# Performance work log

Measured on AMD Instinct MI355X. Metric: run time of the kernel, lower is better.

Reference implementation:

```python
import jax, jax.numpy as jnp
import numpy as np

B, C, N, L = 32, 256, 1024, 12
H = 8
DK = C // H  # 32


def setup_inputs() -> dict:
    key = jax.random.key(0)
    ks = jax.random.split(key, 8)
    inp = {
        "input": jax.random.normal(ks[0], (B, C, N, L), dtype=jnp.float32),
        # 1x1 conv weights stored as [out_ch, in_ch] (kernel is 1x1)
        "q_w": jax.random.normal(ks[1], (C, C), dtype=jnp.float32) * 0.02,
        "q_b": jnp.zeros((C,), dtype=jnp.float32),
        "v_w": jax.random.normal(ks[2], (C, C), dtype=jnp.float32) * 0.02,
        "v_b": jnp.zeros((C,), dtype=jnp.float32),
        "c_w": jax.random.normal(ks[3], (C, C), dtype=jnp.float32) * 0.02,
        "c_b": jnp.zeros((C,), dtype=jnp.float32),
        # xavier_uniform_: bound = sqrt(6/(fan_in+fan_out)) over last two dims
        "s_bank": jax.random.uniform(ks[4], (H, L, N, DK), dtype=jnp.float32,
                                      minval=-1.0, maxval=1.0) * np.float32(np.sqrt(6.0 / (N + DK))),
    }
    return inp


def _conv1x1_relu(x, w, b):
    # x: [B, Cin, N, L], w: [Cout, Cin] -> [B, Cout, N, L]; dropout is eval-mode identity
    return jax.nn.relu(jnp.einsum('oi,binl->bonl', w, x) + b[None, :, None, None])


def reference(input, q_w, q_b, v_w, v_b, c_w, c_b, s_bank):
    b, c, n, l = input.shape
    inv_sqrt_dk = np.float32(1.0 / np.sqrt(DK))

    q = _conv1x1_relu(input, q_w, q_b)   # [B, C, N, L]
    v = _conv1x1_relu(input, v_w, v_b)   # [B, C, N, L]

    def split_heads(t):
        # [B, C, N, L] -> [B, H, DK, N, L] -> [B, H, L, N, DK]
        return t.reshape(b, H, DK, n, l).transpose(0, 1, 4, 3, 2)

    query = jax.nn.softmax(split_heads(q) * inv_sqrt_dk, axis=-1)        # [B,H,L,N,DK]
    value = split_heads(v)                                               # [B,H,L,N,DK]
    key_ = jax.nn.softmax(s_bank[:, :, :n, :] * inv_sqrt_dk, axis=-1)    # [H,L,N,DK]

    kv = jnp.einsum('hlnx,bhlny->bhlxy', key_, value)      # [B,H,L,DK,DK]
    qkv = jnp.einsum('bhlnx,bhlxy->bhlny', query, kv)      # [B,H,L,N,DK]

    # [B,H,L,N,DK] -> [B,H,DK,N,L] -> [B,C,N,L]
    out = qkv.transpose(0, 1, 4, 3, 2).reshape(b, c, n, l)
    return _conv1x1_relu(out, c_w, c_b)
```

## Files before the change

kernel.cpp:

```cpp
#include <hip/hip_runtime.h>

#define B_   32
#define C_   256
#define N_   1024
#define L_   12
#define H_   8
#define DK_  32
#define NL_  12288
#define CNL_ 3145728
#define ND_  32768
#define HLN_ 98304
#define SCALE_ 0.17677669529663687f

typedef _Float16 half8 __attribute__((ext_vector_type(8)));
typedef _Float16 half4 __attribute__((ext_vector_type(4)));
typedef float f32x4 __attribute__((ext_vector_type(4)));

__device__ __forceinline__ int div12(int s) { return (int)(((unsigned)s * 43691u) >> 19); }
__device__ __forceinline__ int fsw(int c) { return c ^ (((c >> 4) & 1) << 2) ^ ((c >> 6) & 3); }

__global__ __launch_bounds__(256) void k_prep_softmax(
    const float* __restrict__ wq, const float* __restrict__ wv,
    const float* __restrict__ cw, const float* __restrict__ sb,
    _Float16* __restrict__ Wfrag, _Float16* __restrict__ Cfrag,
    _Float16* __restrict__ ksT) {
    __shared__ _Float16 smT[32 * 260];
    const int t = threadIdx.x;
    if (blockIdx.x < 96) {
        const int gid = blockIdx.x * 256 + t;
        if (gid < 16384) {
            const int kb = gid >> 11, r = gid & 2047;
            const int mt = r >> 6, o = (r >> 4) & 3, lo = r & 15;
            const int m = mt * 16 + lo;
            const float* src = (m < 256 ? wq + (size_t)m * 256 : wv + (size_t)(m - 256) * 256)
                               + kb * 32 + o * 8;
            f32x4 a0 = *(const f32x4*)src, a1 = *(const f32x4*)(src + 4);
            half8 h;
#pragma unroll
            for (int i = 0; i < 4; ++i) { h[i] = (_Float16)a0[i]; h[4 + i] = (_Float16)a1[i]; }
            *(half8*)(Wfrag + (size_t)gid * 8) = h;
        } else {
            const int c = gid - 16384;
            const int kb = c >> 10, r = c & 1023;
            const int mt = r >> 6, o = (r >> 4) & 3, lo = r & 15;
            const int m = mt * 16 + lo;
            const float* src = cw + (size_t)m * 256 + kb * 32 + o * 8;
            f32x4 a0 = *(const f32x4*)src, a1 = *(const f32x4*)(src + 4);
            half8 h;
#pragma unroll
            for (int i = 0; i < 4; ++i) { h[i] = (_Float16)a0[i]; h[4 + i] = (_Float16)a1[i]; }
            *(half8*)(Cfrag + (size_t)c * 8) = h;
        }
        return;
    }
    const int bx = blockIdx.x - 96;
    const int row = bx * 256 + t;
    const f32x4* src = (const f32x4*)(sb + (size_t)row * DK_);
    float v[DK_];
#pragma unroll
    for (int i = 0; i < 8; i++) {
        f32x4 t4 = src[i];
        v[4*i+0] = t4[0]; v[4*i+1] = t4[1]; v[4*i+2] = t4[2]; v[4*i+3] = t4[3];
    }
    float m = v[0];
#pragma unroll
    for (int i = 1; i < DK_; i++) m = fmaxf(m, v[i]);
    float s = 0.f;
#pragma unroll
    for (int i = 0; i < DK_; i++) { v[i] = __expf((v[i] - m) * SCALE_); s += v[i]; }
    const float inv = 1.f / s;
#pragma unroll
    for (int i = 0; i < DK_; i++) smT[i * 260 + t] = (_Float16)(v[i] * inv);
    __syncthreads();
    const int x = t >> 3, off = (t & 7) * 32;
    const int base = bx * 256;
    const int hl = base >> 10, nb = base & 1023;
    _Float16* dst = ksT + (size_t)hl * ND_ + (size_t)x * 1024 + nb + off;
    const _Float16* srcT = &smT[x * 260 + off];
#pragma unroll
    for (int k = 0; k < 4; ++k)
        *(half8*)(dst + k * 8) = *(const half8*)(srcT + k * 8);
}

__global__ __launch_bounds__(512, 2) void k_conv_qv(
    const float* __restrict__ x, const _Float16* __restrict__ Wfrag,
    const float* __restrict__ bqp, const float* __restrict__ bvp,
    _Float16* __restrict__ qh, _Float16* __restrict__ vh)
{
    __shared__ __align__(16) _Float16 Xl[2][8192];

    const int t = threadIdx.x;
    const int sgrp = blockIdx.x;
    const int b = blockIdx.y;
    const int sbase = sgrp * 768;
    const int w = t >> 6, lane = t & 63;
    const int lo = lane & 15, hi = lane >> 4;

    half8 af[8][4];
#pragma unroll
    for (int kb = 0; kb < 8; ++kb)
#pragma unroll
        for (int m = 0; m < 4; ++m)
            af[kb][m] = *(const half8*)(Wfrag +
                ((size_t)kb*2048 + (size_t)(w*4 + m)*64 + lane) * 8);

    const float* bsel = (w >= 4) ? bvp : bqp;
    f32x4 bb[4];
#pragma unroll
    for (int m = 0; m < 4; ++m)
        bb[m] = *(const f32x4*)(bsel + ((w & 3)*4 + m)*16 + hi*4);

    const int xch = t >> 1, xsh = (t & 1) * 8;
    const int g = xch >> 3, elem = xch & 7;
    const int wb = g*128 + elem;
    const int sx = xsh ^ ((g & 7) << 1) ^ (xsh >> 3);
    const float* px = x + (size_t)b * CNL_ + (size_t)xch * NL_ + sbase + xsh;

    const int base_r = hi*128 + ((lo ^ (hi*2) ^ ((lo & 8) >> 3)) << 3);

    f32x4 c0 = *(const f32x4*)px,        c1 = *(const f32x4*)(px + 4);
    f32x4 c2 = *(const f32x4*)(px + 16), c3 = *(const f32x4*)(px + 20);
#pragma unroll
    for (int k = 0; k < 4; ++k) {
        Xl[0][wb + (((k  ) ^ sx) << 3)]        = (_Float16)c0[k];
        Xl[0][wb + (((k+4) ^ sx) << 3)]        = (_Float16)c1[k];
        Xl[0][4096 + wb + (((k  ) ^ sx) << 3)] = (_Float16)c2[k];
        Xl[0][4096 + wb + (((k+4) ^ sx) << 3)] = (_Float16)c3[k];
    }
    c0 = *(const f32x4*)(px + 32); c1 = *(const f32x4*)(px + 36);
    c2 = *(const f32x4*)(px + 48); c3 = *(const f32x4*)(px + 52);

    for (int i = 0; i < 24; ++i) {
        asm volatile("s_waitcnt lgkmcnt(0)" ::: "memory");
        __builtin_amdgcn_s_barrier();
        __builtin_amdgcn_sched_barrier(0);
        if (i < 23) {
            _Float16* Xn = Xl[(i + 1) & 1];
#pragma unroll
            for (int k = 0; k < 4; ++k) {
                Xn[wb + (((k  ) ^ sx) << 3)]        = (_Float16)c0[k];
                Xn[wb + (((k+4) ^ sx) << 3)]        = (_Float16)c1[k];
                Xn[4096 + wb + (((k  ) ^ sx) << 3)] = (_Float16)c2[k];
                Xn[4096 + wb + (((k+4) ^ sx) << 3)] = (_Float16)c3[k];
            }
            if (i < 22) {
                const float* p = px + (size_t)(i + 2) * 32;
                c0 = *(const f32x4*)p;        c1 = *(const f32x4*)(p + 4);
                c2 = *(const f32x4*)(p + 16); c3 = *(const f32x4*)(p + 20);
            }
        }
        const _Float16* Xc = Xl[i & 1];
        f32x4 acc[4][2] = {};
#pragma unroll
        for (int kb = 0; kb < 8; ++kb) {
            const int ro = kb*512 + (base_r ^ ((kb & 1) << 6));
            half8 bf0 = *(const half8*)&Xc[ro];
            half8 bf1 = *(const half8*)&Xc[4096 + ro];
#pragma unroll
            for (int m = 0; m < 4; ++m) {
                acc[m][0] = __builtin_amdgcn_mfma_f32_16x16x32_f16(af[kb][m], bf0, acc[m][0], 0, 0, 0);
                acc[m][1] = __builtin_amdgcn_mfma_f32_16x16x32_f16(af[kb][m], bf1, acc[m][1], 0, 0, 0);
            }
        }
#pragma unroll
        for (int u = 0; u < 2; ++u) {
            const int sg = sbase + i*32 + u*16 + lo;
            const int n = div12(sg), l = sg - n*12;
#pragma unroll
            for (int m = 0; m < 4; ++m) {
                const int o = (w*4 + m)*16 + hi*4;
                const int ol = o & 255;
                _Float16* dst0 = (w >= 4) ? vh : qh;
                half4 hh;
#pragma unroll
                for (int r = 0; r < 4; ++r) hh[r] = (_Float16)fmaxf(acc[m][u][r] + bb[m][r], 0.f);
                *(half4*)(dst0 + ((size_t)(b*8 + (ol >> 5))*12 + l)*ND_ + (size_t)n*32 + (ol & 31)) = hh;
            }
        }
    }
}

__global__ __launch_bounds__(256) void k_kv(const _Float16* __restrict__ ksT,
    const _Float16* __restrict__ v, _Float16* __restrict__ kvT) {
    __shared__ float red[4096];
    const int bid = blockIdx.x;
    const int bh = bid / 12;
    const int l  = bid - bh * 12;
    const int h  = bh & 7;
    const int t = threadIdx.x, w = t >> 6, lane = t & 63;
    const int lo = lane & 15, hi = lane >> 4;
    const _Float16* vb  = v   + (size_t)bid * ND_;
    const _Float16* ksb = ksT + (size_t)(h*12 + l) * ND_;

    f32x4 acc[2][2] = {};
#pragma unroll 2
    for (int c = 0; c < 8; ++c) {
        const int n0 = w*256 + c*32 + hi*8;
        half8 a0, a1;
#pragma unroll
        for (int j = 0; j < 8; ++j) {
            a0[j] = vb[(size_t)(n0 + j)*32 + lo];
            a1[j] = vb[(size_t)(n0 + j)*32 + 16 + lo];
        }
        half8 b0 = *(const half8*)(ksb + (size_t)lo*1024 + n0);
        half8 b1 = *(const half8*)(ksb + (size_t)(16 + lo)*1024 + n0);
        acc[0][0] = __builtin_amdgcn_mfma_f32_16x16x32_f16(a0, b0, acc[0][0], 0, 0, 0);
        acc[0][1] = __builtin_amdgcn_mfma_f32_16x16x32_f16(a0, b1, acc[0][1], 0, 0, 0);
        acc[1][0] = __builtin_amdgcn_mfma_f32_16x16x32_f16(a1, b0, acc[1][0], 0, 0, 0);
        acc[1][1] = __builtin_amdgcn_mfma_f32_16x16x32_f16(a1, b1, acc[1][1], 0, 0, 0);
    }
#pragma unroll
    for (int m = 0; m < 2; ++m)
#pragma unroll
        for (int xm = 0; xm < 2; ++xm)
#pragma unroll
            for (int reg = 0; reg < 4; ++reg)
                red[w*1024 + (m*16 + hi*4 + reg)*32 + xm*16 + lo] = acc[m][xm][reg];
    __syncthreads();
    const int e = t * 4;
    f32x4 s = *(const f32x4*)&red[e];
    s += *(const f32x4*)&red[1024 + e];
    s += *(const f32x4*)&red[2048 + e];
    s += *(const f32x4*)&red[3072 + e];
    half4 o;
#pragma unroll
    for (int i = 0; i < 4; ++i) o[i] = (_Float16)s[i];
    *(half4*)(kvT + (size_t)bid * 1024 + e) = o;
}

__global__ __launch_bounds__(512, 2) void k_conv_out(
    const _Float16* __restrict__ q, const _Float16* __restrict__ kvw,
    const _Float16* __restrict__ Cfrag, const float* __restrict__ cbp,
    float* __restrict__ out) {
    __shared__ __align__(16) _Float16 Xt[2][6144];
    __shared__ float Cb[256];

    const int t = threadIdx.x;
    const int bx = blockIdx.x, b = blockIdx.y;
    const int s0 = bx * 192;
    const int n0 = bx * 16;
    const int w = t >> 6, lane = t & 63;
    const int lo = lane & 15, hi = lane >> 4;
    if (t < 64) *(f32x4*)&Cb[t*4] = *(const f32x4*)(cbp + t*4);

    f32x4 acc[4][6] = {};

    const bool pvw = (w < 6);
    const int li0 = w * 2;
    const int qrow = n0 + lo;
    const size_t hstep = (size_t)12 * ND_;
    const _Float16* qb_b = q + (size_t)b * 8 * hstep;
    const _Float16* kv_b = kvw + (size_t)b * 98304;

    half8 hq0 = {}, hq1 = {};
    if (pvw) {
        hq0 = *(const half8*)(qb_b + (size_t)li0 * ND_ + (size_t)qrow*32 + hi*8);
        hq1 = *(const half8*)(qb_b + (size_t)(li0+1) * ND_ + (size_t)qrow*32 + hi*8);
    }

    for (int ph = 0; ph <= 8; ++ph) {
        if (ph < 8 && pvw) {
            half8 nq0 = hq0, nq1 = hq1;
            if (ph < 7) {
                nq0 = *(const half8*)(qb_b + (ph+1)*hstep + (size_t)li0 * ND_ + (size_t)qrow*32 + hi*8);
                nq1 = *(const half8*)(qb_b + (ph+1)*hstep + (size_t)(li0+1) * ND_ + (size_t)qrow*32 + hi*8);
            }
            const _Float16* kvh = kv_b + (size_t)ph * 12288;
            _Float16* Xd = Xt[ph & 1];
#pragma unroll
            for (int sub = 0; sub < 2; ++sub) {
                const half8 hq = sub ? hq1 : hq0;
                const int li = li0 + sub;
                float qv[8];
#pragma unroll
                for (int i = 0; i < 8; ++i) qv[i] = (float)hq[i];
                float m8 = fmaxf(fmaxf(fmaxf(qv[0], qv[1]), fmaxf(qv[2], qv[3])),
                                 fmaxf(fmaxf(qv[4], qv[5]), fmaxf(qv[6], qv[7])));
                m8 = fmaxf(m8, __shfl_xor(m8, 16));
                m8 = fmaxf(m8, __shfl_xor(m8, 32));
                const float mS = m8 * SCALE_;
                float ex[8]; float ssum = 0.f;
#pragma unroll
                for (int i = 0; i < 8; ++i) { ex[i] = __expf(qv[i]*SCALE_ - mS); ssum += ex[i]; }
                ssum += __shfl_xor(ssum, 16);
                ssum += __shfl_xor(ssum, 32);
                const float pin = 1.f / ssum;
                half8 af;
#pragma unroll
                for (int i = 0; i < 8; ++i) af[i] = (_Float16)(ex[i] * pin);
                const half8 b0 = *(const half8*)(kvh + li*1024 + lo*32 + hi*8);
                const half8 b1 = *(const half8*)(kvh + li*1024 + (16+lo)*32 + hi*8);
                f32x4 d0 = {}, d1 = {};
                d0 = __builtin_amdgcn_mfma_f32_16x16x32_f16(af, b0, d0, 0, 0, 0);
                d1 = __builtin_amdgcn_mfma_f32_16x16x32_f16(af, b1, d1, 0, 0, 0);
#pragma unroll
                for (int reg = 0; reg < 4; ++reg) {
                    const int sr = (hi*4 + reg)*12 + li;
                    const int cb_ = (sr >> 4)*64 + (sr & 15);
                    const int ca = cb_ + (lo >> 3)*16;
                    const int cc = cb_ + (2 + (lo >> 3))*16;
                    Xd[fsw(ca)*8 + (lo & 7)] = (_Float16)d0[reg];
                    Xd[fsw(cc)*8 + (lo & 7)] = (_Float16)d1[reg];
                }
            }
            hq0 = nq0; hq1 = nq1;
        }
        if (ph >= 1) {
            const _Float16* Wk = Cfrag + (size_t)(ph - 1) * 8192;
            const _Float16* Xc = Xt[(ph - 1) & 1];
            half8 af2[4], bf[6];
#pragma unroll
            for (int m = 0; m < 4; ++m)
                af2[m] = *(const half8*)(Wk + ((((w>>1)*4 + m)*4 + hi)*16 + lo) * 8);
#pragma unroll
            for (int sf = 0; sf < 6; ++sf) {
                const int rc = ((w & 1)*6 + sf)*64 + hi*16 + lo;
                bf[sf] = *(const half8*)&Xc[fsw(rc)*8];
            }
#pragma unroll
            for (int m = 0; m < 4; ++m)
#pragma unroll
                for (int sf = 0; sf < 6; ++sf)
                    acc[m][sf] = __builtin_amdgcn_mfma_f32_16x16x32_f16(af2[m], bf[sf], acc[m][sf], 0, 0, 0);
        }
        asm volatile("s_waitcnt lgkmcnt(0)" ::: "memory");
        __builtin_amdgcn_s_barrier();
        __builtin_amdgcn_sched_barrier(0);
    }

#pragma unroll
    for (int m = 0; m < 4; ++m) {
        const int o = (w>>1)*64 + m*16 + hi*4;
        const f32x4 bb = *(const f32x4*)&Cb[o];
#pragma unroll
        for (int sf = 0; sf < 6; ++sf) {
            const int s = s0 + (w&1)*96 + sf*16 + lo;
            float* dst = out + (size_t)(b*256 + o)*12288 + s;
#pragma unroll
            for (int i = 0; i < 4; ++i)
                dst[(size_t)i * 12288] = fmaxf(acc[m][sf][i] + bb[i], 0.f);
        }
    }
}

extern "C" void kernel_launch(void* const* d_in, const int* in_sizes, int n_in,
                              void* d_out, int out_size, void* d_ws, size_t ws_size,
                              hipStream_t stream) {
    const float* input = (const float*)d_in[0];
    const float* q_w   = (const float*)d_in[1];
    const float* q_b   = (const float*)d_in[2];
    const float* v_w   = (const float*)d_in[3];
    const float* v_b   = (const float*)d_in[4];
    const float* c_w   = (const float*)d_in[5];
    const float* c_b   = (const float*)d_in[6];
    const float* s_bank= (const float*)d_in[7];
    float* out = (float*)d_out;

    char* ws = (char*)d_ws;
    _Float16* ks16 = (_Float16*)ws;
    _Float16* qh   = (_Float16*)(ws + 6291456);
    _Float16* vh   = qh + (size_t)100663296;
    _Float16* kvT  = vh + (size_t)100663296;
    _Float16* Wfrag= kvT + (size_t)3145728;
    _Float16* Cfrag= Wfrag + (size_t)131072;

    k_prep_softmax<<<dim3(96 + HLN_/256), dim3(256), 0, stream>>>(
        q_w, v_w, c_w, s_bank, Wfrag, Cfrag, ks16);
    k_conv_qv<<<dim3(16, 32), dim3(512), 0, stream>>>(input, Wfrag, q_b, v_b, qh, vh);
    k_kv<<<dim3(B_ * H_ * L_), dim3(256), 0, stream>>>(ks16, vh, kvT);
    k_conv_out<<<dim3(64, 32), dim3(512), 0, stream>>>(qh, kvT, Cfrag, c_b, out);
}
```

Baseline: 528.9 us.

## Deepen conv_qv global prefetch to two stages and give each kv wave its own slice

In the q/v projection kernel, global loads of the input tile are issued two iterations ahead, using two register sets that alternate with a 2x-unrolled loop, instead of one iteration ahead. The aim is to hide more global memory latency behind the MFMA work. In the kv kernel, each wave now computes a whole (b,h,l) slice across all of N, which removes the shared-memory cross-wave reduction and the __syncthreads. The grid shrinks to a quarter, and each wave writes its result directly with scattered half stores; the cost is more registers in conv_qv and longer serial loops per wave in kv.

```diff
diff --git a/kernel.cpp b/kernel.cpp
--- a/kernel.cpp
+++ b/kernel.cpp
@@ -118,35 +118,55 @@
 
     const int base_r = hi*128 + ((lo ^ (hi*2) ^ ((lo & 8) >> 3)) << 3);
 
-    f32x4 c0 = *(const f32x4*)px,        c1 = *(const f32x4*)(px + 4);
-    f32x4 c2 = *(const f32x4*)(px + 16), c3 = *(const f32x4*)(px + 20);
-#pragma unroll
-    for (int k = 0; k < 4; ++k) {
-        Xl[0][wb + (((k  ) ^ sx) << 3)]        = (_Float16)c0[k];
-        Xl[0][wb + (((k+4) ^ sx) << 3)]        = (_Float16)c1[k];
-        Xl[0][4096 + wb + (((k  ) ^ sx) << 3)] = (_Float16)c2[k];
-        Xl[0][4096 + wb + (((k+4) ^ sx) << 3)] = (_Float16)c3[k];
-    }
-    c0 = *(const f32x4*)(px + 32); c1 = *(const f32x4*)(px + 36);
-    c2 = *(const f32x4*)(px + 48); c3 = *(const f32x4*)(px + 52);
-
+    {
+        f32x4 t0 = *(const f32x4*)px,        t1 = *(const f32x4*)(px + 4);
+        f32x4 t2 = *(const f32x4*)(px + 16), t3 = *(const f32x4*)(px + 20);
+#pragma unroll
+        for (int k = 0; k < 4; ++k) {
+            Xl[0][wb + (((k  ) ^ sx) << 3)]        = (_Float16)t0[k];
+            Xl[0][wb + (((k+4) ^ sx) << 3)]        = (_Float16)t1[k];
+            Xl[0][4096 + wb + (((k  ) ^ sx) << 3)] = (_Float16)t2[k];
+            Xl[0][4096 + wb + (((k+4) ^ sx) << 3)] = (_Float16)t3[k];
+        }
+    }
+    f32x4 cB0 = *(const f32x4*)(px + 32), cB1 = *(const f32x4*)(px + 36);
+    f32x4 cB2 = *(const f32x4*)(px + 48), cB3 = *(const f32x4*)(px + 52);
+    f32x4 cA0 = *(const f32x4*)(px + 64), cA1 = *(const f32x4*)(px + 68);
+    f32x4 cA2 = *(const f32x4*)(px + 80), cA3 = *(const f32x4*)(px + 84);
+
+#pragma unroll 2
     for (int i = 0; i < 24; ++i) {
         asm volatile("s_waitcnt lgkmcnt(0)" ::: "memory");
         __builtin_amdgcn_s_barrier();
         __builtin_amdgcn_sched_barrier(0);
         if (i < 23) {
             _Float16* Xn = Xl[(i + 1) & 1];
-#pragma unroll
-            for (int k = 0; k < 4; ++k) {
-                Xn[wb + (((k  ) ^ sx) << 3)]        = (_Float16)c0[k];
-                Xn[wb + (((k+4) ^ sx) << 3)]        = (_Float16)c1[k];
-                Xn[4096 + wb + (((k  ) ^ sx) << 3)] = (_Float16)c2[k];
-                Xn[4096 + wb + (((k+4) ^ sx) << 3)] = (_Float16)c3[k];
-            }
-            if (i < 22) {
-                const float* p = px + (size_t)(i + 2) * 32;
-                c0 = *(const f32x4*)p;        c1 = *(const f32x4*)(p + 4);
-                c2 = *(const f32x4*)(p + 16); c3 = *(const f32x4*)(p + 20);
+            if ((i + 1) & 1) {
+#pragma unroll
+                for (int k = 0; k < 4; ++k) {
+                    Xn[wb + (((k  ) ^ sx) << 3)]        = (_Float16)cB0[k];
+                    Xn[wb + (((k+4) ^ sx) << 3)]        = (_Float16)cB1[k];
+                    Xn[4096 + wb + (((k  ) ^ sx) << 3)] = (_Float16)cB2[k];
+                    Xn[4096 + wb + (((k+4) ^ sx) << 3)] = (_Float16)cB3[k];
+                }
+                if (i < 21) {
+                    const float* p = px + (size_t)(i + 3) * 32;
+                    cB0 = *(const f32x4*)p;        cB1 = *(const f32x4*)(p + 4);
+                    cB2 = *(const f32x4*)(p + 16); cB3 = *(const f32x4*)(p + 20);
+                }
+            } else {
+#pragma unroll
+                for (int k = 0; k < 4; ++k) {
+                    Xn[wb + (((k  ) ^ sx) << 3)]        = (_Float16)cA0[k];
+                    Xn[wb + (((k+4) ^ sx) << 3)]        = (_Float16)cA1[k];
+                    Xn[4096 + wb + (((k  ) ^ sx) << 3)] = (_Float16)cA2[k];
+                    Xn[4096 + wb + (((k+4) ^ sx) << 3)] = (_Float16)cA3[k];
+                }
+                if (i < 21) {
+                    const float* p = px + (size_t)(i + 3) * 32;
+                    cA0 = *(const f32x4*)p;        cA1 = *(const f32x4*)(p + 4);
+                    cA2 = *(const f32x4*)(p + 16); cA3 = *(const f32x4*)(p + 20);
+                }
             }
         }
         const _Float16* Xc = Xl[i & 1];
@@ -182,20 +202,20 @@
 
 __global__ __launch_bounds__(256) void k_kv(const _Float16* __restrict__ ksT,
     const _Float16* __restrict__ v, _Float16* __restrict__ kvT) {
-    __shared__ float red[4096];
-    const int bid = blockIdx.x;
+    const int t = threadIdx.x;
+    const int wv = t >> 6, lane = t & 63;
+    const int bid = blockIdx.x * 4 + wv;
     const int bh = bid / 12;
     const int l  = bid - bh * 12;
     const int h  = bh & 7;
-    const int t = threadIdx.x, w = t >> 6, lane = t & 63;
     const int lo = lane & 15, hi = lane >> 4;
     const _Float16* vb  = v   + (size_t)bid * ND_;
     const _Float16* ksb = ksT + (size_t)(h*12 + l) * ND_;
 
     f32x4 acc[2][2] = {};
-#pragma unroll 2
-    for (int c = 0; c < 8; ++c) {
-        const int n0 = w*256 + c*32 + hi*8;
+#pragma unroll 4
+    for (int c = 0; c < 32; ++c) {
+        const int n0 = c*32 + hi*8;
         half8 a0, a1;
 #pragma unroll
         for (int j = 0; j < 8; ++j) {
@@ -209,23 +229,14 @@
         acc[1][0] = __builtin_amdgcn_mfma_f32_16x16x32_f16(a1, b0, acc[1][0], 0, 0, 0);
         acc[1][1] = __builtin_amdgcn_mfma_f32_16x16x32_f16(a1, b1, acc[1][1], 0, 0, 0);
     }
+    _Float16* dst = kvT + (size_t)bid * 1024;
 #pragma unroll
     for (int m = 0; m < 2; ++m)
 #pragma unroll
         for (int xm = 0; xm < 2; ++xm)
 #pragma unroll
             for (int reg = 0; reg < 4; ++reg)
-                red[w*1024 + (m*16 + hi*4 + reg)*32 + xm*16 + lo] = acc[m][xm][reg];
-    __syncthreads();
-    const int e = t * 4;
-    f32x4 s = *(const f32x4*)&red[e];
-    s += *(const f32x4*)&red[1024 + e];
-    s += *(const f32x4*)&red[2048 + e];
-    s += *(const f32x4*)&red[3072 + e];
-    half4 o;
-#pragma unroll
-    for (int i = 0; i < 4; ++i) o[i] = (_Float16)s[i];
-    *(half4*)(kvT + (size_t)bid * 1024 + e) = o;
+                dst[(m*16 + hi*4 + reg)*32 + xm*16 + lo] = (_Float16)acc[m][xm][reg];
 }
 
 __global__ __launch_bounds__(512, 2) void k_conv_out(
@@ -367,6 +378,6 @@
     k_prep_softmax<<<dim3(96 + HLN_/256), dim3(256), 0, stream>>>(
         q_w, v_w, c_w, s_bank, Wfrag, Cfrag, ks16);
     k_conv_qv<<<dim3(16, 32), dim3(512), 0, stream>>>(input, Wfrag, q_b, v_b, qh, vh);
-    k_kv<<<dim3(B_ * H_ * L_), dim3(256), 0, stream>>>(ks16, vh, kvT);
+    k_kv<<<dim3(B_ * H_ * L_ / 4), dim3(256), 0, stream>>>(ks16, vh, kvT);
     k_conv_out<<<dim3(64, 32), dim3(512), 0, stream>>>(qh, kvT, Cfrag, c_b, out);
 }
```

Result: faster. 515.8 us (-2.5%).
